# Kernel tuning notes

Hardware: AMD Instinct MI355X
Metric: run time of the kernel (lower is better)

Reference implementation:

```python
import jax, jax.numpy as jnp
import numpy as np

BS, NV, T, SD = 128, 32, 128, 64  # groups, observed vars, timesteps, state dim


def setup_inputs() -> dict:
    key = jax.random.key(0)
    k1, k2, k3, k4, k5 = jax.random.split(key, 5)
    x = jax.random.normal(k1, (BS, NV, T), jnp.float32)
    # Stable transition matrix (spectral radius < 1 so 128-step recursion is well-behaved)
    F = 0.3 * jnp.eye(SD, dtype=jnp.float32) + 0.05 * jax.random.normal(k2, (SD, SD), jnp.float32)
    H = jax.random.normal(k3, (NV, SD), jnp.float32) / jnp.sqrt(SD).astype(jnp.float32)
    A = jax.random.normal(k4, (NV, NV), jnp.float32)
    R = A @ A.T / NV + jnp.eye(NV, dtype=jnp.float32)          # SPD observation noise
    B = jax.random.normal(k5, (SD, SD), jnp.float32)
    Q = 0.1 * (B @ B.T) / SD + 0.01 * jnp.eye(SD, dtype=jnp.float32)  # SPD process noise
    return {"x": x, "F": F, "H": H, "R": R, "Q": Q}


def _kf_forward(x, F, H, R, Q):
    """forward() == predict_ahead(x, n_ahead=1) squeezed: [bs, nv, T]."""
    bs, nv, T_ = x.shape
    sd = F.shape[0]
    I = jnp.eye(sd, dtype=x.dtype)
    m0 = jnp.zeros((bs, sd), x.dtype)               # initializer: zero mean
    P0 = jnp.broadcast_to(I, (bs, sd, sd))          # initializer: identity covariance
    obs_seq = jnp.moveaxis(x, 2, 0)[: T_ - 1]       # [T-1, bs, nv]
    Ft, Ht = F.T, H.T

    def step(carry, o):
        m, P = carry                                # m: [bs,sd], P: [bs,sd,sd]
        # --- update ---
        PHt = P @ Ht                                # [bs, sd, nv]
        S = jnp.matmul(H, PHt) + R                  # [bs, nv, nv]
        resid = o - m @ Ht                          # [bs, nv]
        Sinv = jnp.linalg.inv(S)                    # batched inverse
        K = PHt @ Sinv                              # [bs, sd, nv]
        m_u = m + jnp.einsum('bsv,bv->bs', K, resid)
        p1 = I - jnp.matmul(K, H)                   # [bs, sd, sd]
        # Joseph stabilized covariance update
        P_u = p1 @ P @ p1.swapaxes(-1, -2) + (K @ R) @ K.swapaxes(-1, -2)
        # --- predict (n_ahead = 1) ---
        m_p = m_u @ Ft                              # (F @ m)
        P_p = jnp.matmul(F, P_u) @ Ft + Q
        y = m_p @ Ht                                # [bs, nv] -> output[:, :, i+1]
        return (m_p, P_p), y

    _, ys = jax.lax.scan(step, (m0, P0), obs_seq)   # ys: [T-1, bs, nv]
    out = jnp.concatenate([jnp.zeros((1, bs, nv), x.dtype), ys], axis=0)  # t=0 stays zero
    return jnp.moveaxis(out, 0, 2)                  # [bs, nv, T]


def reference(x, F, H, R, Q):
    return _kf_forward(x, F, H, R, Q)
```

## Files before the change

### kernel.cpp

```cpp
#include <hip/hip_runtime.h>


#define SD 64
#define NV 32
#define TSZ 128
#define BSZ 128
#define TMAX 120

#define MG_STRIDE (SD*SD + SD*NV)
#define WS_PAIR (120*MG_STRIDE)
#define WS_TC   (WS_PAIR + 27648)
#define OFF_M2   0
#define OFF_M3   4096
#define OFF_M4   8192
#define OFF_MG   12288
#define OFF_M2G  14336
#define OFF_M3G  16384
#define OFF_HM   18432
#define OFF_HM2  20480
#define OFF_HM3  22528
#define OFF_HG   24576
#define OFF_HMG  25600
#define OFF_HM2G 26624

#define AFB    0
#define APB    4352
#define AWB    8704
#define AHB    13056
#define AHTB   15232
#define AGRB   17536
#define AVB    19840
#define AYB    22144
#define ASIP   24320
#define ATF    25472
#define ASF    29632
#define APREVG 30688
#define AWRED  32800
#define ASZ    32808

typedef __attribute__((ext_vector_type(8))) short bf16x8;
typedef __attribute__((ext_vector_type(4))) float f32x4;

__device__ __forceinline__ unsigned packhl(float v) {
  unsigned b = __float_as_uint(v);
  unsigned hi = (b + 0x7FFFu + ((b >> 16) & 1u)) & 0xFFFF0000u;
  float lo = v - __uint_as_float(hi);
  unsigned lb = __float_as_uint(lo);
  unsigned lo16 = ((lb + 0x7FFFu + ((lb >> 16) & 1u)) >> 16);
  return hi | (lo16 & 0xFFFFu);
}

__device__ __forceinline__ void frags_from(const unsigned* __restrict__ p,
                                           bf16x8& hi, bf16x8& lo) {
  uint4 a = *(const uint4*)p;
  uint4 b = *(const uint4*)(p + 4);
  unsigned u0=a.x,u1=a.y,u2=a.z,u3=a.w,u4=b.x,u5=b.y,u6=b.z,u7=b.w;
  hi[0]=(short)(u0>>16); hi[1]=(short)(u1>>16); hi[2]=(short)(u2>>16); hi[3]=(short)(u3>>16);
  hi[4]=(short)(u4>>16); hi[5]=(short)(u5>>16); hi[6]=(short)(u6>>16); hi[7]=(short)(u7>>16);
  lo[0]=(short)(u0&0xFFFFu); lo[1]=(short)(u1&0xFFFFu); lo[2]=(short)(u2&0xFFFFu); lo[3]=(short)(u3&0xFFFFu);
  lo[4]=(short)(u4&0xFFFFu); lo[5]=(short)(u5&0xFFFFu); lo[6]=(short)(u6&0xFFFFu); lo[7]=(short)(u7&0xFFFFu);
}
// ... 12 lines not shown
__device__ __forceinline__ float rdlane(float v, int lane) {
  return __uint_as_float(
      (unsigned)__builtin_amdgcn_readlane((int)__float_as_uint(v), lane));
}

__device__ const int DE0[5][8] = {
  {APB, AWB, OFF_M2, 64, 2, 16, AFB,  1},
  {AWB, APB, -1,     64, 2, 16, AHTB, 1},
  {APB, AYB, OFF_MG, 32, 1, 8,  ATF,  2},
  {AHB, AWB, OFF_HM, 64, 2, 8,  AVB,  1},
  {AHB, AYB, OFF_HG, 32, 1, 4,  -1,   0},
};
__device__ const int DE1[8][8] = {
  {AFB, AWB,  OFF_M3,   64, 2, 16, -1, 0},
  {AFB, AHTB, OFF_M4,   64, 2, 16, -1, 0},
  {AFB, AYB,  OFF_M2G,  32, 1, 8,  -1, 0},
  {AFB, ATF,  OFF_M3G,  32, 1, 8,  -1, 0},
  {AVB, AWB,  OFF_HM2,  64, 2, 8,  -1, 0},
  {AVB, AHTB, OFF_HM3,  64, 2, 8,  -1, 0},
  {AVB, AYB,  OFF_HMG,  32, 1, 4,  -1, 0},
  {AVB, ATF,  OFF_HM2G, 32, 1, 4,  -1, 0},
};

__device__ __forceinline__ void run_desc(const int (*D)[8], int nD, int totT,
                                         unsigned* U, float* M2o,
                                         int w, int l16, int quad) {
  for (int gt = w; gt < totT; gt += 8) {
    int ti = gt, di = 0;
    while (ti >= D[di][5]) { ti -= D[di][5]; ++di; }
    const int* d = D[di];
    const int nTs = d[4];
    const int m0 = (ti >> nTs) << 4, n0 = (ti & ((1 << nTs) - 1)) << 4;
    f32x4 c = {0.f, 0.f, 0.f, 0.f};
    const unsigned* ap = U + d[0] + (m0 + l16) * 68 + quad * 8;
    const unsigned* bp = U + d[1] + (n0 + l16) * 68 + quad * 8;
    c = mfma3(ap, bp, c);
    c = mfma3(ap + 32, bp + 32, c);
    const int r0 = m0 + quad * 4, cc = n0 + l16;
    if (d[2] >= 0) {
#pragma unroll
      for (int g = 0; g < 4; ++g) M2o[d[2] + (r0 + g) * d[3] + cc] = c[g];
    }
    if (d[7] == 1) {
#pragma unroll
      for (int g = 0; g < 4; ++g) U[d[6] + (r0 + g) * 68 + cc] = packhl(c[g]);
    } else if (d[7] == 2) {
      *(uint4*)(U + d[6] + cc * 68 + r0) =
          make_uint4(packhl(c[0]), packhl(c[1]), packhl(c[2]), packhl(c[3]));
    }
  }
}

__launch_bounds__(512)
__global__ void kf_phase1(const float* __restrict__ Fg,
                          const float* __restrict__ Hg,
                          const float* __restrict__ Rg,
                          const float* __restrict__ Qg,
                          float* __restrict__ ws) {
  __shared__ unsigned AR[ASZ];
  unsigned* U = AR;
  float* Ff = (float*)AR;

  const int tid = threadIdx.x;
  const int w = tid >> 6, lane = tid & 63, quad = lane >> 4, l16 = lane & 15;

  for (int s = tid; s < SD*SD; s += 512) {
    int i = s >> 6, j = s & 63;
    U[AFB + i*68 + j] = packhl(Fg[s]);
    U[APB + i*68 + j] = packhl((i == j) ? 1.0f : 0.0f);
  }
  for (int s = tid; s < NV*SD; s += 512)
    U[AHB + (s>>6)*68 + (s&63)] = packhl(Hg[s]);
  for (int s = tid; s < SD*NV; s += 512) {
    int j = s >> 5, v = s & 31;
    U[AHTB + j*36 + v] = packhl(Hg[v*SD + j]);
    Ff[APREVG + j*33 + v] = 1e30f;
  }
  __syncthreads();

  int tcv = TMAX - 1;

  for (int t = 0; t < TMAX; ++t) {
    float* Mws = ws + (size_t)t * MG_STRIDE;
    float* Gws = Mws + SD*SD;

    for (int tt = w; tt < 24; tt += 8) {
      if (tt < 8) {
        const int m0 = (tt >> 2) << 4, n0 = (tt & 3) << 4;
        f32x4 c = {0.f, 0.f, 0.f, 0.f};
        c = mfma3(U + AHB + (m0+l16)*68 +      quad*8, U + APB + (n0+l16)*68 +      quad*8, c);
        c = mfma3(U + AHB + (m0+l16)*68 + 32 + quad*8, U + APB + (n0+l16)*68 + 32 + quad*8, c);
        const int r0 = m0 + quad*4, cc = n0 + l16;
        U[AYB + (r0+0)*68 + cc] = packhl(c[0]);
        U[AYB + (r0+1)*68 + cc] = packhl(c[1]);
        U[AYB + (r0+2)*68 + cc] = packhl(c[2]);
        U[AYB + (r0+3)*68 + cc] = packhl(c[3]);
      } else {
        const int ss = tt - 8;
        const int m0 = (ss >> 2) << 4, n0 = (ss & 3) << 4;
        f32x4 c = {0.f, 0.f, 0.f, 0.f};
        c = mfma3(U + AFB + (m0+l16)*68 +      quad*8, U + APB + (n0+l16)*68 +      quad*8, c);
        c = mfma3(U + AFB + (m0+l16)*68 + 32 + quad*8, U + APB + (n0+l16)*68 + 32 + quad*8, c);
        const int r0 = m0 + quad*4, cc = n0 + l16;
        U[AWB + (r0+0)*68 + cc] = packhl(c[0]);
        U[AWB + (r0+1)*68 + cc] = packhl(c[1]);
        U[AWB + (r0+2)*68 + cc] = packhl(c[2]);
        U[AWB + (r0+3)*68 + cc] = packhl(c[3]);
      }
    }
    __syncthreads();

    for (int tt = w; tt < 12; tt += 8) {
      if (tt < 4) {
        const int m0 = (tt >> 1) << 4, n0 = (tt & 1) << 4;
        const int r0 = m0 + quad*4, cc = n0 + l16;
        f32x4 c;
        c[0] = Rg[(r0+0)*NV + cc];
        c[1] = Rg[(r0+1)*NV + cc];
        c[2] = Rg[(r0+2)*NV + cc];
        c[3] = Rg[(r0+3)*NV + cc];
        c = mfma3(U + AYB + (m0+l16)*68 +      quad*8, U + AHB + (n0+l16)*68 +      quad*8, c);
        c = mfma3(U + AYB + (m0+l16)*68 + 32 + quad*8, U + AHB + (n0+l16)*68 + 32 + quad*8, c);
        Ff[ASF + (r0+0)*33 + cc] = c[0];
        Ff[ASF + (r0+1)*33 + cc] = c[1];
        Ff[ASF + (r0+2)*33 + cc] = c[2];
        Ff[ASF + (r0+3)*33 + cc] = c[3];
      } else {
        const int ss = tt - 4;
        const int m0 = (ss >> 1) << 4, n0 = (ss & 1) << 4;
        f32x4 c = {0.f, 0.f, 0.f, 0.f};
        c = mfma3(U + AWB + (m0+l16)*68 +      quad*8, U + AHB + (n0+l16)*68 +      quad*8, c);
        c = mfma3(U + AWB + (m0+l16)*68 + 32 + quad*8, U + AHB + (n0+l16)*68 + 32 + quad*8, c);
        const int r0 = m0 + quad*4, cc = n0 + l16;
        U[AVB + (r0+0)*36 + cc] = packhl(c[0]);
        U[AVB + (r0+1)*36 + cc] = packhl(c[1]);
        U[AVB + (r0+2)*36 + cc] = packhl(c[2]);
        U[AVB + (r0+3)*36 + cc] = packhl(c[3]);
      }
    }
    __syncthreads();

    if (tid < 64) {
      const int l = tid;
      float colX[32];
      if (l < 32) {
#pragma unroll
        for (int r = 0; r < 32; ++r) colX[r] = Ff[ASF + r*33 + l];
      } else {
#pragma unroll
        for (int r = 0; r < 32; ++r) colX[r] = (r == l - 32) ? 1.0f : 0.0f;
      }
#pragma unroll
      for (int p = 0; p < 32; ++p) {
        const float piv = rdlane(colX[p], p);
        float inv = __builtin_amdgcn_rcpf(piv);
        inv = inv * (2.0f - piv * inv);
        const float rp = colX[p] * inv;
#pragma unroll
        for (int r = 0; r < 32; ++r) {
          if (r == p) continue;
          const float f = rdlane(colX[r], p);
          colX[r] -= f * rp;
        }
        colX[p] = rp;
      }
      if (l >= 32) {
        const int c = l - 32;
#pragma unroll
        for (int r = 0; r < 32; ++r)
          U[ASIP + r*36 + c] = packhl(colX[r]);
      }
    } else {
      for (int tt = w - 1; tt < 16; tt += 7) {
        const int m0 = (tt >> 2) << 4, n0 = (tt & 3) << 4;
        f32x4 c = {0.f, 0.f, 0.f, 0.f};
        c = mfma3(U + AWB + (m0+l16)*68 +      quad*8, U + AFB + (n0+l16)*68 +      quad*8, c);
        c = mfma3(U + AWB + (m0+l16)*68 + 32 + quad*8, U + AFB + (n0+l16)*68 + 32 + quad*8, c);
        const int r0 = m0 + quad*4, cc = n0 + l16;
        Ff[ATF + (r0+0)*65 + cc] = c[0];
        Ff[ATF + (r0+1)*65 + cc] = c[1];
        Ff[ATF + (r0+2)*65 + cc] = c[2];
        Ff[ATF + (r0+3)*65 + cc] = c[3];
      }
    }
    __syncthreads();

    {
      const int m0 = (w >> 1) << 4, n0 = (w & 1) << 4;
      f32x4 c = {0.f, 0.f, 0.f, 0.f};
      c = mfma3(U + AVB + (m0+l16)*36 + quad*8, U + ASIP + (n0+l16)*36 + quad*8, c);
      const int r0 = m0 + quad*4, cc = n0 + l16;
      float dmax = 0.0f;
#pragma unroll
      for (int g = 0; g < 4; ++g) {
        const float gv = c[g];
        Gws[(r0+g)*NV + cc] = gv;
        U[AGRB + (r0+g)*36 + cc] = packhl(-gv);
        dmax = fmaxf(dmax, fabsf(gv - Ff[APREVG + (r0+g)*33 + cc]));
        Ff[APREVG + (r0+g)*33 + cc] = gv;
      }
#pragma unroll
      for (int off = 32; off >= 1; off >>= 1)
        dmax = fmaxf(dmax, __shfl_xor(dmax, off));
      if (lane == 0) Ff[AWRED + w] = dmax;
    }
    __syncthreads();

    for (int tt = w; tt < 32; tt += 8) {
      if (tt < 16) {
        const int m0 = (tt >> 2) << 4, n0 = (tt & 3) << 4;
        const int r0 = m0 + quad*4, cc = n0 + l16;
        f32x4 c;
        c[0] = Fg[(r0+0)*SD + cc];
        c[1] = Fg[(r0+1)*SD + cc];
        c[2] = Fg[(r0+2)*SD + cc];
        c[3] = Fg[(r0+3)*SD + cc];
        c = mfma3(U + AGRB + (m0+l16)*36 + quad*8, U + AHTB + (n0+l16)*36 + quad*8, c);
        Mws[(r0+0)*SD + cc] = c[0];
        Mws[(r0+1)*SD + cc] = c[1];
        Mws[(r0+2)*SD + cc] = c[2];
        Mws[(r0+3)*SD + cc] = c[3];
      } else {
        const int ss = tt - 16;
        const int m0 = (ss >> 2) << 4, n0 = (ss & 3) << 4;
        const int r0 = m0 + quad*4, cc = n0 + l16;
        f32x4 c;
        c[0] = Ff[ATF + (r0+0)*65 + cc] + Qg[(r0+0)*SD + cc];
        c[1] = Ff[ATF + (r0+1)*65 + cc] + Qg[(r0+1)*SD + cc];
        c[2] = Ff[ATF + (r0+2)*65 + cc] + Qg[(r0+2)*SD + cc];
        c[3] = Ff[ATF + (r0+3)*65 + cc] + Qg[(r0+3)*SD + cc];
        c = mfma3(U + AGRB + (m0+l16)*36 + quad*8, U + AVB + (n0+l16)*36 + quad*8, c);
        U[APB + (r0+0)*68 + cc] = packhl(c[0]);
        U[APB + (r0+1)*68 + cc] = packhl(c[1]);
        U[APB + (r0+2)*68 + cc] = packhl(c[2]);
        U[APB + (r0+3)*68 + cc] = packhl(c[3]);
      }
    }
    __syncthreads();

    float cm = Ff[AWRED + 0];
#pragma unroll
    for (int k = 1; k < 8; ++k) cm = fmaxf(cm, Ff[AWRED + k]);
    if (cm < 3e-4f) { tcv = t; break; }
  }
  if (tid == 0) ((int*)ws)[WS_TC] = tcv;

  {
    const float* Mf = ws + (size_t)tcv * MG_STRIDE;
    const float* Gf = Mf + SD*SD;
    for (int s = tid; s < SD*SD; s += 512) {
      int i = s >> 6, j = s & 63;
      unsigned pk = packhl(Mf[s]);
      U[APB + i*68 + j] = pk;
      U[AWB + j*68 + i] = pk;
    }
    for (int s = tid; s < SD*NV; s += 512) {
      int i = s >> 5, v = s & 31;
      U[AYB + v*68 + i] = packhl(Gf[s]);
    }
    __syncthreads();
    float* M2o = ws + WS_PAIR;
    run_desc(DE0, 5, 52, U, M2o, w, l16, quad);
    __syncthreads();
    run_desc(DE1, 8, 72, U, M2o, w, l16, quad);
  }
}

__launch_bounds__(256)
__global__ void kf_phase2(const float* __restrict__ x,
                          const float* __restrict__ Hg,
                          const float* __restrict__ ws,
                          float* __restrict__ out) {
  __shared__ __align__(16) float Hs2[NV*65];
  __shared__ __align__(16) float xt[132*36];
  __shared__ __align__(16) float yb[NV*129];
  __shared__ __align__(16) float mbuf[2*SD];
  __shared__ __align__(16) float M4s [SD*68];
  __shared__ __align__(16) float M3Gs[SD*36];
  __shared__ __align__(16) float M2Gs[SD*36];
  __shared__ __align__(16) float MGs [SD*36];
  __shared__ __align__(16) float Gs  [SD*36];
  __shared__ __align__(16) float HMs [NV*68];
  __shared__ __align__(16) float HM2s[NV*68];
  __shared__ __align__(16) float HM3s[NV*68];
  __shared__ __align__(16) float HGs [NV*36];
  __shared__ __align__(16) float HMGs[NV*36];
  __shared__ __align__(16) float HM2Gs[NV*36];
  const int tid = threadIdx.x, b = blockIdx.x;

  const int tc = ((const int*)ws)[WS_TC];
  const float* P = ws + WS_PAIR;
  const float* Gf = ws + (size_t)tc * MG_STRIDE + SD*SD;

  for (int s = tid; s < NV*SD; s += 256) {
    int v = s >> 6, j = s & 63;
    Hs2[v*65 + j] = Hg[s];
    HMs [v*68 + j] = P[OFF_HM  + s];
    HM2s[v*68 + j] = P[OFF_HM2 + s];
    HM3s[v*68 + j] = P[OFF_HM3 + s];
  }
  for (int s = tid; s < SD*SD; s += 256) M4s[(s>>6)*68 + (s&63)] = P[OFF_M4 + s];
  for (int s = tid; s < SD*NV; s += 256) {
    int i = s >> 5, v = s & 31;
    M3Gs[i*36 + v] = P[OFF_M3G + s];
    M2Gs[i*36 + v] = P[OFF_M2G + s];
    MGs [i*36 + v] = P[OFF_MG  + s];
    Gs  [i*36 + v] = Gf[s];
  }
  for (int s = tid; s < NV*NV; s += 256) {
    int v = s >> 5, u = s & 31;
    HGs  [v*36 + u] = P[OFF_HG   + s];
    HMGs [v*36 + u] = P[OFF_HMG  + s];
    HM2Gs[v*36 + u] = P[OFF_HM2G + s];
  }
  for (int s = tid; s < 4*36; s += 256) xt[128*36 + s] = 0.0f;
  for (int s = tid; s < NV*TSZ; s += 256) {
    int v = s >> 7, t = s & 127;
    xt[t*36 + v] = x[(size_t)b*NV*TSZ + s];
  }
  if (tid < NV) yb[tid*129] = 0.0f;
  if (tid < 2*SD) mbuf[tid] = 0.0f;
  __syncthreads();

  const int i = tid >> 2, p4 = tid & 3;
  const int v = tid >> 3, p8 = tid & 7;
  int cb = 0;

  for (int t = 0; t < tc; ++t) {
    const float* Mt = ws + (size_t)t * MG_STRIDE;
    const float* Gt = Mt + SD*SD;
    const float* cur = mbuf + cb * SD;
    float*       nxt = mbuf + (cb ^ 1) * SD;

    float acc = 0.0f;
    {
      const int j0 = p4 * 16;
#pragma unroll
      for (int c = 0; c < 16; c += 4) {
        float4 mm = *(const float4*)(Mt + i*SD + j0 + c);
        float4 vv = *(const float4*)(cur + j0 + c);
        acc += mm.x*vv.x + mm.y*vv.y + mm.z*vv.z + mm.w*vv.w;
      }
      const int v0 = p4 * 8;
#pragma unroll
      for (int c = 0; c < 8; c += 4) {
        float4 gg = *(const float4*)(Gt + i*NV + v0 + c);
        float4 oo = *(const float4*)(xt + t*36 + v0 + c);
        acc += gg.x*oo.x + gg.y*oo.y + gg.z*oo.z + gg.w*oo.w;
      }
    }
    acc += __shfl_xor(acc, 1);
    acc += __shfl_xor(acc, 2);

    if (t >= 1) {
      float ys = 0.0f;
#pragma unroll
      for (int j = 0; j < 8; ++j)
        ys += Hs2[v*65 + p8*8 + j] * cur[p8*8 + j];
      ys += __shfl_xor(ys, 1);
      ys += __shfl_xor(ys, 2);
      ys += __shfl_xor(ys, 4);
      if (p8 == 0) yb[v*129 + t] = ys;
    }
    if (p4 == 0) nxt[i] = acc;
    __syncthreads();
    cb ^= 1;
  }

  for (int t = tc; t < TSZ; t += 4) {
    const float* cur = mbuf + cb * SD;
    float*       nxt = mbuf + (cb ^ 1) * SD;
    const float* o0 = xt + t*36;
    const float* o1 = o0 + 36;
    const float* o2 = o1 + 36;
    const float* o3 = o2 + 36;

    {
      const int j8 = p8 * 8, j4 = p8 * 4;
      float y0 = 0.f, y1 = 0.f, y2 = 0.f, y3 = 0.f;
#pragma unroll
      for (int c = 0; c < 8; c += 4) {
        float4 vv = *(const float4*)(cur + j8 + c);
        float4 h0 = *(const float4*)(Hs2 + v*65 + j8 + c);
        float4 h1 = *(const float4*)(HMs + v*68 + j8 + c);
        float4 h2 = *(const float4*)(HM2s + v*68 + j8 + c);
        float4 h3 = *(const float4*)(HM3s + v*68 + j8 + c);
        y0 += h0.x*vv.x + h0.y*vv.y + h0.z*vv.z + h0.w*vv.w;
        y1 += h1.x*vv.x + h1.y*vv.y + h1.z*vv.z + h1.w*vv.w;
        y2 += h2.x*vv.x + h2.y*vv.y + h2.z*vv.z + h2.w*vv.w;
        y3 += h3.x*vv.x + h3.y*vv.y + h3.z*vv.z + h3.w*vv.w;
      }
      {
        float4 a = *(const float4*)(HGs + v*36 + j4);
        float4 bq = *(const float4*)(HMGs + v*36 + j4);
        float4 cq = *(const float4*)(HM2Gs + v*36 + j4);
        float4 q0 = *(const float4*)(o0 + j4);
        float4 q1 = *(const float4*)(o1 + j4);
        float4 q2 = *(const float4*)(o2 + j4);
        y1 += a.x*q0.x + a.y*q0.y + a.z*q0.z + a.w*q0.w;
        y2 += bq.x*q0.x + bq.y*q0.y + bq.z*q0.z + bq.w*q0.w
            + a.x*q1.x + a.y*q1.y + a.z*q1.z + a.w*q1.w;
        y3 += cq.x*q0.x + cq.y*q0.y + cq.z*q0.z + cq.w*q0.w
            + bq.x*q1.x + bq.y*q1.y + bq.z*q1.z + bq.w*q1.w
            + a.x*q2.x + a.y*q2.y + a.z*q2.z + a.w*q2.w;
      }
#pragma unroll
      for (int off = 1; off <= 4; off <<= 1) {
        y0 += __shfl_xor(y0, off);
        y1 += __shfl_xor(y1, off);
        y2 += __shfl_xor(y2, off);
        y3 += __shfl_xor(y3, off);
      }
      if (p8 == 0) {
        yb[v*129 + t] = y0;
        if (t + 1 < TSZ) yb[v*129 + t + 1] = y1;
        if (t + 2 < TSZ) yb[v*129 + t + 2] = y2;
        if (t + 3 < TSZ) yb[v*129 + t + 3] = y3;
      }
    }

    {
      float acc = 0.0f;
      const int j0 = p4 * 16;
#pragma unroll
      for (int c = 0; c < 16; c += 4) {
        float4 mm = *(const float4*)(M4s + i*68 + j0 + c);
        float4 vv = *(const float4*)(cur + j0 + c);
        acc += mm.x*vv.x + mm.y*vv.y + mm.z*vv.z + mm.w*vv.w;
      }
      const int v0 = p4 * 8;
#pragma unroll
      for (int c = 0; c < 8; c += 4) {
        float4 g3 = *(const float4*)(M3Gs + i*36 + v0 + c);
        float4 g2 = *(const float4*)(M2Gs + i*36 + v0 + c);
        float4 g1 = *(const float4*)(MGs + i*36 + v0 + c);
        float4 g0 = *(const float4*)(Gs + i*36 + v0 + c);
        float4 q0 = *(const float4*)(o0 + v0 + c);
        float4 q1 = *(const float4*)(o1 + v0 + c);
        float4 q2 = *(const float4*)(o2 + v0 + c);
        float4 q3 = *(const float4*)(o3 + v0 + c);
        acc += g3.x*q0.x + g3.y*q0.y + g3.z*q0.z + g3.w*q0.w;
        acc += g2.x*q1.x + g2.y*q1.y + g2.z*q1.z + g2.w*q1.w;
        acc += g1.x*q2.x + g1.y*q2.y + g1.z*q2.z + g1.w*q2.w;
        acc += g0.x*q3.x + g0.y*q3.y + g0.z*q3.z + g0.w*q3.w;
      }
      acc += __shfl_xor(acc, 1);
      acc += __shfl_xor(acc, 2);
      if (p4 == 0) nxt[i] = acc;
    }
    __syncthreads();
    cb ^= 1;
  }

  for (int s = tid; s < NV*TSZ; s += 256)
    out[(size_t)b*NV*TSZ + s] = yb[(s>>7)*129 + (s&127)];
}

extern "C" void kernel_launch(void* const* d_in, const int* in_sizes, int n_in,
                              void* d_out, int out_size, void* d_ws, size_t ws_size,
                              hipStream_t stream) {
  const float* x = (const float*)d_in[0];
  const float* F = (const float*)d_in[1];
  const float* H = (const float*)d_in[2];
  const float* R = (const float*)d_in[3];
  const float* Q = (const float*)d_in[4];
  float* out = (float*)d_out;
  float* ws  = (float*)d_ws;

  hipLaunchKernelGGL(kf_phase1, dim3(1), dim3(512), 0, stream, F, H, R, Q, ws);
  hipLaunchKernelGGL(kf_phase2, dim3(BSZ), dim3(256), 0, stream, x, H, ws, out);
}
```

Measured before the change: 199.3 us.

## Fuse gain-precompute and batch filter kernels with flag-based producer-consumer overlap

Merges the single-block covariance/gain kernel and the per-batch mean-recursion kernel into one launch of 129 blocks. Block 0 computes the gain sequence and publishes progress through a release-store flag in workspace, while the other 128 blocks spin on that flag and consume each step's M/G as soon as it is written. This overlaps the serial Riccati recursion with the batch mean updates and removes a kernel launch boundary. It relies on all 129 blocks being co-resident to avoid deadlock, and it adds spin-wait and global fence overhead. The Gauss-Jordan inverse loop is also reworked to a rotating-register form with unroll 1, which shrinks code size.

```diff
diff --git a/kernel.cpp b/kernel.cpp
--- a/kernel.cpp
+++ b/kernel.cpp
@@ -4,12 +4,11 @@
 #define SD 64
 #define NV 32
 #define TSZ 128
-#define BSZ 128
 #define TMAX 120
 
 #define MG_STRIDE (SD*SD + SD*NV)
 #define WS_PAIR (120*MG_STRIDE)
-#define WS_TC   (WS_PAIR + 27648)
+#define WS_FLAG (WS_PAIR + 27648)
 #define OFF_M2   0
 #define OFF_M3   4096
 #define OFF_M4   8192
@@ -36,7 +35,24 @@
 #define ASF    29632
 #define APREVG 30688
 #define AWRED  32800
-#define ASZ    32808
+
+#define P2_HS2  0
+#define P2_XT   2080
+#define P2_YB   6832
+#define P2_MB   10960
+#define P2_M4   11088
+#define P2_M3G  15440
+#define P2_M2G  17744
+#define P2_MG   20048
+#define P2_G    22352
+#define P2_HM   24656
+#define P2_HM2  26832
+#define P2_HM3  29008
+#define P2_HG   31184
+#define P2_HMG  32336
+#define P2_HM2G 33488
+#define P2_FLG  34640
+#define ASZ2    34644
 
 typedef __attribute__((ext_vector_type(8))) short bf16x8;
 typedef __attribute__((ext_vector_type(4))) float f32x4;
@@ -95,7 +111,7 @@
   {AVB, ATF,  OFF_HM2G, 32, 1, 4,  -1, 0},
 };
 
-__device__ __forceinline__ void run_desc(const int (*D)[8], int nD, int totT,
+__device__ __forceinline__ void run_desc(const int (*D)[8], int totT,
                                          unsigned* U, float* M2o,
                                          int w, int l16, int quad) {
   for (int gt = w; gt < totT; gt += 8) {
@@ -125,408 +141,428 @@
 }
 
 __launch_bounds__(512)
-__global__ void kf_phase1(const float* __restrict__ Fg,
-                          const float* __restrict__ Hg,
-                          const float* __restrict__ Rg,
-                          const float* __restrict__ Qg,
-                          float* __restrict__ ws) {
-  __shared__ unsigned AR[ASZ];
-  unsigned* U = AR;
-  float* Ff = (float*)AR;
-
+__global__ void kf_fused(const float* __restrict__ x,
+                         const float* __restrict__ Fg,
+                         const float* __restrict__ Hg,
+                         const float* __restrict__ Rg,
+                         const float* __restrict__ Qg,
+                         float* __restrict__ out,
+                         float* __restrict__ ws) {
+  __shared__ unsigned AR[ASZ2];
   const int tid = threadIdx.x;
   const int w = tid >> 6, lane = tid & 63, quad = lane >> 4, l16 = lane & 15;
-
-  for (int s = tid; s < SD*SD; s += 512) {
-    int i = s >> 6, j = s & 63;
-    U[AFB + i*68 + j] = packhl(Fg[s]);
-    U[APB + i*68 + j] = packhl((i == j) ? 1.0f : 0.0f);
-  }
-  for (int s = tid; s < NV*SD; s += 512)
-    U[AHB + (s>>6)*68 + (s&63)] = packhl(Hg[s]);
-  for (int s = tid; s < SD*NV; s += 512) {
-    int j = s >> 5, v = s & 31;
-    U[AHTB + j*36 + v] = packhl(Hg[v*SD + j]);
-    Ff[APREVG + j*33 + v] = 1e30f;
-  }
-  __syncthreads();
-
-  int tcv = TMAX - 1;
-
-  for (int t = 0; t < TMAX; ++t) {
-    float* Mws = ws + (size_t)t * MG_STRIDE;
-    float* Gws = Mws + SD*SD;
-
-    for (int tt = w; tt < 24; tt += 8) {
-      if (tt < 8) {
-        const int m0 = (tt >> 2) << 4, n0 = (tt & 3) << 4;
-        f32x4 c = {0.f, 0.f, 0.f, 0.f};
-        c = mfma3(U + AHB + (m0+l16)*68 +      quad*8, U + APB + (n0+l16)*68 +      quad*8, c);
-        c = mfma3(U + AHB + (m0+l16)*68 + 32 + quad*8, U + APB + (n0+l16)*68 + 32 + quad*8, c);
-        const int r0 = m0 + quad*4, cc = n0 + l16;
-        U[AYB + (r0+0)*68 + cc] = packhl(c[0]);
-        U[AYB + (r0+1)*68 + cc] = packhl(c[1]);
-        U[AYB + (r0+2)*68 + cc] = packhl(c[2]);
-        U[AYB + (r0+3)*68 + cc] = packhl(c[3]);
-      } else {
-        const int ss = tt - 8;
-        const int m0 = (ss >> 2) << 4, n0 = (ss & 3) << 4;
-        f32x4 c = {0.f, 0.f, 0.f, 0.f};
-        c = mfma3(U + AFB + (m0+l16)*68 +      quad*8, U + APB + (n0+l16)*68 +      quad*8, c);
-        c = mfma3(U + AFB + (m0+l16)*68 + 32 + quad*8, U + APB + (n0+l16)*68 + 32 + quad*8, c);
-        const int r0 = m0 + quad*4, cc = n0 + l16;
-        U[AWB + (r0+0)*68 + cc] = packhl(c[0]);
-        U[AWB + (r0+1)*68 + cc] = packhl(c[1]);
-        U[AWB + (r0+2)*68 + cc] = packhl(c[2]);
-        U[AWB + (r0+3)*68 + cc] = packhl(c[3]);
-      }
-    }
-    __syncthreads();
-
-    for (int tt = w; tt < 12; tt += 8) {
-      if (tt < 4) {
-        const int m0 = (tt >> 1) << 4, n0 = (tt & 1) << 4;
-        const int r0 = m0 + quad*4, cc = n0 + l16;
-        f32x4 c;
-        c[0] = Rg[(r0+0)*NV + cc];
-        c[1] = Rg[(r0+1)*NV + cc];
-        c[2] = Rg[(r0+2)*NV + cc];
-        c[3] = Rg[(r0+3)*NV + cc];
-        c = mfma3(U + AYB + (m0+l16)*68 +      quad*8, U + AHB + (n0+l16)*68 +      quad*8, c);
-        c = mfma3(U + AYB + (m0+l16)*68 + 32 + quad*8, U + AHB + (n0+l16)*68 + 32 + quad*8, c);
-        Ff[ASF + (r0+0)*33 + cc] = c[0];
-        Ff[ASF + (r0+1)*33 + cc] = c[1];
-        Ff[ASF + (r0+2)*33 + cc] = c[2];
-        Ff[ASF + (r0+3)*33 + cc] = c[3];
-      } else {
-        const int ss = tt - 4;
-        const int m0 = (ss >> 1) << 4, n0 = (ss & 1) << 4;
-        f32x4 c = {0.f, 0.f, 0.f, 0.f};
-        c = mfma3(U + AWB + (m0+l16)*68 +      quad*8, U + AHB + (n0+l16)*68 +      quad*8, c);
-        c = mfma3(U + AWB + (m0+l16)*68 + 32 + quad*8, U + AHB + (n0+l16)*68 + 32 + quad*8, c);
-        const int r0 = m0 + quad*4, cc = n0 + l16;
-        U[AVB + (r0+0)*36 + cc] = packhl(c[0]);
-        U[AVB + (r0+1)*36 + cc] = packhl(c[1]);
-        U[AVB + (r0+2)*36 + cc] = packhl(c[2]);
-        U[AVB + (r0+3)*36 + cc] = packhl(c[3]);
-      }
-    }
-    __syncthreads();
-
-    if (tid < 64) {
-      const int l = tid;
-      float colX[32];
-      if (l < 32) {
-#pragma unroll
-        for (int r = 0; r < 32; ++r) colX[r] = Ff[ASF + r*33 + l];
-      } else {
-#pragma unroll
-        for (int r = 0; r < 32; ++r) colX[r] = (r == l - 32) ? 1.0f : 0.0f;
-      }
-#pragma unroll
-      for (int p = 0; p < 32; ++p) {
-        const float piv = rdlane(colX[p], p);
-        float inv = __builtin_amdgcn_rcpf(piv);
-        inv = inv * (2.0f - piv * inv);
-        const float rp = colX[p] * inv;
-#pragma unroll
-        for (int r = 0; r < 32; ++r) {
-          if (r == p) continue;
-          const float f = rdlane(colX[r], p);
-          colX[r] -= f * rp;
-        }
-        colX[p] = rp;
-      }
-      if (l >= 32) {
-        const int c = l - 32;
-#pragma unroll
-        for (int r = 0; r < 32; ++r)
-          U[ASIP + r*36 + c] = packhl(colX[r]);
-      }
-    } else {
-      for (int tt = w - 1; tt < 16; tt += 7) {
-        const int m0 = (tt >> 2) << 4, n0 = (tt & 3) << 4;
-        f32x4 c = {0.f, 0.f, 0.f, 0.f};
-        c = mfma3(U + AWB + (m0+l16)*68 +      quad*8, U + AFB + (n0+l16)*68 +      quad*8, c);
-        c = mfma3(U + AWB + (m0+l16)*68 + 32 + quad*8, U + AFB + (n0+l16)*68 + 32 + quad*8, c);
-        const int r0 = m0 + quad*4, cc = n0 + l16;
-        Ff[ATF + (r0+0)*65 + cc] = c[0];
-        Ff[ATF + (r0+1)*65 + cc] = c[1];
-        Ff[ATF + (r0+2)*65 + cc] = c[2];
-        Ff[ATF + (r0+3)*65 + cc] = c[3];
-      }
-    }
-    __syncthreads();
-
-    {
-      const int m0 = (w >> 1) << 4, n0 = (w & 1) << 4;
-      f32x4 c = {0.f, 0.f, 0.f, 0.f};
-      c = mfma3(U + AVB + (m0+l16)*36 + quad*8, U + ASIP + (n0+l16)*36 + quad*8, c);
-      const int r0 = m0 + quad*4, cc = n0 + l16;
-      float dmax = 0.0f;
-#pragma unroll
-      for (int g = 0; g < 4; ++g) {
-        const float gv = c[g];
-        Gws[(r0+g)*NV + cc] = gv;
-        U[AGRB + (r0+g)*36 + cc] = packhl(-gv);
-        dmax = fmaxf(dmax, fabsf(gv - Ff[APREVG + (r0+g)*33 + cc]));
-        Ff[APREVG + (r0+g)*33 + cc] = gv;
-      }
-#pragma unroll
-      for (int off = 32; off >= 1; off >>= 1)
-        dmax = fmaxf(dmax, __shfl_xor(dmax, off));
-      if (lane == 0) Ff[AWRED + w] = dmax;
-    }
-    __syncthreads();
-
-    for (int tt = w; tt < 32; tt += 8) {
-      if (tt < 16) {
-        const int m0 = (tt >> 2) << 4, n0 = (tt & 3) << 4;
-        const int r0 = m0 + quad*4, cc = n0 + l16;
-        f32x4 c;
-        c[0] = Fg[(r0+0)*SD + cc];
-        c[1] = Fg[(r0+1)*SD + cc];
-        c[2] = Fg[(r0+2)*SD + cc];
-        c[3] = Fg[(r0+3)*SD + cc];
-        c = mfma3(U + AGRB + (m0+l16)*36 + quad*8, U + AHTB + (n0+l16)*36 + quad*8, c);
-        Mws[(r0+0)*SD + cc] = c[0];
-        Mws[(r0+1)*SD + cc] = c[1];
-        Mws[(r0+2)*SD + cc] = c[2];
-        Mws[(r0+3)*SD + cc] = c[3];
-      } else {
-        const int ss = tt - 16;
-        const int m0 = (ss >> 2) << 4, n0 = (ss & 3) << 4;
-        const int r0 = m0 + quad*4, cc = n0 + l16;
-        f32x4 c;
-        c[0] = Ff[ATF + (r0+0)*65 + cc] + Qg[(r0+0)*SD + cc];
-        c[1] = Ff[ATF + (r0+1)*65 + cc] + Qg[(r0+1)*SD + cc];
-        c[2] = Ff[ATF + (r0+2)*65 + cc] + Qg[(r0+2)*SD + cc];
-        c[3] = Ff[ATF + (r0+3)*65 + cc] + Qg[(r0+3)*SD + cc];
-        c = mfma3(U + AGRB + (m0+l16)*36 + quad*8, U + AVB + (n0+l16)*36 + quad*8, c);
-        U[APB + (r0+0)*68 + cc] = packhl(c[0]);
-        U[APB + (r0+1)*68 + cc] = packhl(c[1]);
-        U[APB + (r0+2)*68 + cc] = packhl(c[2]);
-        U[APB + (r0+3)*68 + cc] = packhl(c[3]);
-      }
-    }
-    __syncthreads();
-
-    float cm = Ff[AWRED + 0];
-#pragma unroll
-    for (int k = 1; k < 8; ++k) cm = fmaxf(cm, Ff[AWRED + k]);
-    if (cm < 3e-4f) { tcv = t; break; }
-  }
-  if (tid == 0) ((int*)ws)[WS_TC] = tcv;
-
-  {
-    const float* Mf = ws + (size_t)tcv * MG_STRIDE;
-    const float* Gf = Mf + SD*SD;
+  int* flagp = (int*)ws + WS_FLAG;
+
+  if (blockIdx.x == 0) {
+    unsigned* U = AR;
+    float* Ff = (float*)AR;
+
     for (int s = tid; s < SD*SD; s += 512) {
       int i = s >> 6, j = s & 63;
-      unsigned pk = packhl(Mf[s]);
-      U[APB + i*68 + j] = pk;
-      U[AWB + j*68 + i] = pk;
-    }
+      U[AFB + i*68 + j] = packhl(Fg[s]);
+      U[APB + i*68 + j] = packhl((i == j) ? 1.0f : 0.0f);
+    }
+    for (int s = tid; s < NV*SD; s += 512)
+      U[AHB + (s>>6)*68 + (s&63)] = packhl(Hg[s]);
     for (int s = tid; s < SD*NV; s += 512) {
-      int i = s >> 5, v = s & 31;
-      U[AYB + v*68 + i] = packhl(Gf[s]);
+      int j = s >> 5, v = s & 31;
+      U[AHTB + j*36 + v] = packhl(Hg[v*SD + j]);
+      Ff[APREVG + j*33 + v] = 1e30f;
     }
     __syncthreads();
-    float* M2o = ws + WS_PAIR;
-    run_desc(DE0, 5, 52, U, M2o, w, l16, quad);
+
+    int tcv = TMAX - 1;
+
+    for (int t = 0; t < TMAX; ++t) {
+      float* Mws = ws + (size_t)t * MG_STRIDE;
+      float* Gws = Mws + SD*SD;
+
+      for (int tt = w; tt < 24; tt += 8) {
+        if (tt < 8) {
+          const int m0 = (tt >> 2) << 4, n0 = (tt & 3) << 4;
+          f32x4 c = {0.f, 0.f, 0.f, 0.f};
+          c = mfma3(U + AHB + (m0+l16)*68 +      quad*8, U + APB + (n0+l16)*68 +      quad*8, c);
+          c = mfma3(U + AHB + (m0+l16)*68 + 32 + quad*8, U + APB + (n0+l16)*68 + 32 + quad*8, c);
+          const int r0 = m0 + quad*4, cc = n0 + l16;
+          U[AYB + (r0+0)*68 + cc] = packhl(c[0]);
+          U[AYB + (r0+1)*68 + cc] = packhl(c[1]);
+          U[AYB + (r0+2)*68 + cc] = packhl(c[2]);
+          U[AYB + (r0+3)*68 + cc] = packhl(c[3]);
+        } else {
+          const int ss = tt - 8;
+          const int m0 = (ss >> 2) << 4, n0 = (ss & 3) << 4;
+          f32x4 c = {0.f, 0.f, 0.f, 0.f};
+          c = mfma3(U + AFB + (m0+l16)*68 +      quad*8, U + APB + (n0+l16)*68 +      quad*8, c);
+          c = mfma3(U + AFB + (m0+l16)*68 + 32 + quad*8, U + APB + (n0+l16)*68 + 32 + quad*8, c);
+          const int r0 = m0 + quad*4, cc = n0 + l16;
+          U[AWB + (r0+0)*68 + cc] = packhl(c[0]);
+          U[AWB + (r0+1)*68 + cc] = packhl(c[1]);
+          U[AWB + (r0+2)*68 + cc] = packhl(c[2]);
+          U[AWB + (r0+3)*68 + cc] = packhl(c[3]);
+        }
+      }
+      __syncthreads();
+
+      for (int tt = w; tt < 12; tt += 8) {
+        if (tt < 4) {
+          const int m0 = (tt >> 1) << 4, n0 = (tt & 1) << 4;
+          const int r0 = m0 + quad*4, cc = n0 + l16;
+          f32x4 c;
+          c[0] = Rg[(r0+0)*NV + cc];
+          c[1] = Rg[(r0+1)*NV + cc];
+          c[2] = Rg[(r0+2)*NV + cc];
+          c[3] = Rg[(r0+3)*NV + cc];
+          c = mfma3(U + AYB + (m0+l16)*68 +      quad*8, U + AHB + (n0+l16)*68 +      quad*8, c);
+          c = mfma3(U + AYB + (m0+l16)*68 + 32 + quad*8, U + AHB + (n0+l16)*68 + 32 + quad*8, c);
+          Ff[ASF + (r0+0)*33 + cc] = c[0];
+          Ff[ASF + (r0+1)*33 + cc] = c[1];
+          Ff[ASF + (r0+2)*33 + cc] = c[2];
+          Ff[ASF + (r0+3)*33 + cc] = c[3];
+        } else {
+          const int ss = tt - 4;
+          const int m0 = (ss >> 1) << 4, n0 = (ss & 1) << 4;
+          f32x4 c = {0.f, 0.f, 0.f, 0.f};
+          c = mfma3(U + AWB + (m0+l16)*68 +      quad*8, U + AHB + (n0+l16)*68 +      quad*8, c);
+          c = mfma3(U + AWB + (m0+l16)*68 + 32 + quad*8, U + AHB + (n0+l16)*68 + 32 + quad*8, c);
+          const int r0 = m0 + quad*4, cc = n0 + l16;
+          U[AVB + (r0+0)*36 + cc] = packhl(c[0]);
+          U[AVB + (r0+1)*36 + cc] = packhl(c[1]);
+          U[AVB + (r0+2)*36 + cc] = packhl(c[2]);
+          U[AVB + (r0+3)*36 + cc] = packhl(c[3]);
+        }
+      }
+      __syncthreads();
+
+      if (tid < 64) {
+        const int l = tid;
+        float cur[32];
+        if (l < 32) {
+#pragma unroll
+          for (int r = 0; r < 32; ++r) cur[r] = Ff[ASF + r*33 + l];
+        } else {
+#pragma unroll
+          for (int r = 0; r < 32; ++r) cur[r] = (r == l - 32) ? 1.0f : 0.0f;
+        }
+#pragma unroll 1
+        for (int p = 0; p < 32; ++p) {
+          const float piv = rdlane(cur[0], p);
+          float inv = __builtin_amdgcn_rcpf(piv);
+          inv = inv * (2.0f - piv * inv);
+          const float rp = cur[0] * inv;
+#pragma unroll
+          for (int r = 1; r < 32; ++r) {
+            const float f = rdlane(cur[r], p);
+            cur[r-1] = cur[r] - f * rp;
+          }
+          cur[31] = rp;
+        }
+        if (l >= 32) {
+          const int c = l - 32;
+#pragma unroll
+          for (int r = 0; r < 32; ++r)
+            U[ASIP + r*36 + c] = packhl(cur[r]);
+        }
+      } else {
+        for (int tt = w - 1; tt < 16; tt += 7) {
+          const int m0 = (tt >> 2) << 4, n0 = (tt & 3) << 4;
+          f32x4 c = {0.f, 0.f, 0.f, 0.f};
+          c = mfma3(U + AWB + (m0+l16)*68 +      quad*8, U + AFB + (n0+l16)*68 +      quad*8, c);
+          c = mfma3(U + AWB + (m0+l16)*68 + 32 + quad*8, U + AFB + (n0+l16)*68 + 32 + quad*8, c);
+          const int r0 = m0 + quad*4, cc = n0 + l16;
+          Ff[ATF + (r0+0)*65 + cc] = c[0];
+          Ff[ATF + (r0+1)*65 + cc] = c[1];
+          Ff[ATF + (r0+2)*65 + cc] = c[2];
+          Ff[ATF + (r0+3)*65 + cc] = c[3];
+        }
+      }
+      __syncthreads();
+
+      {
+        const int m0 = (w >> 1) << 4, n0 = (w & 1) << 4;
+        f32x4 c = {0.f, 0.f, 0.f, 0.f};
+        c = mfma3(U + AVB + (m0+l16)*36 + quad*8, U + ASIP + (n0+l16)*36 + quad*8, c);
+        const int r0 = m0 + quad*4, cc = n0 + l16;
+        float dmax = 0.0f;
+#pragma unroll
+        for (int g = 0; g < 4; ++g) {
+          const float gv = c[g];
+          Gws[(r0+g)*NV + cc] = gv;
+          U[AGRB + (r0+g)*36 + cc] = packhl(-gv);
+          dmax = fmaxf(dmax, fabsf(gv - Ff[APREVG + (r0+g)*33 + cc]));
+          Ff[APREVG + (r0+g)*33 + cc] = gv;
+        }
+#pragma unroll
+        for (int off = 32; off >= 1; off >>= 1)
+          dmax = fmaxf(dmax, __shfl_xor(dmax, off));
+        if (lane == 0) Ff[AWRED + w] = dmax;
+      }
+      __syncthreads();
+
+      for (int tt = w; tt < 32; tt += 8) {
+        if (tt < 16) {
+          const int m0 = (tt >> 2) << 4, n0 = (tt & 3) << 4;
+          const int r0 = m0 + quad*4, cc = n0 + l16;
+          f32x4 c;
+          c[0] = Fg[(r0+0)*SD + cc];
+          c[1] = Fg[(r0+1)*SD + cc];
+          c[2] = Fg[(r0+2)*SD + cc];
+          c[3] = Fg[(r0+3)*SD + cc];
+          c = mfma3(U + AGRB + (m0+l16)*36 + quad*8, U + AHTB + (n0+l16)*36 + quad*8, c);
+          Mws[(r0+0)*SD + cc] = c[0];
+          Mws[(r0+1)*SD + cc] = c[1];
+          Mws[(r0+2)*SD + cc] = c[2];
+          Mws[(r0+3)*SD + cc] = c[3];
+        } else {
+          const int ss = tt - 16;
+          const int m0 = (ss >> 2) << 4, n0 = (ss & 3) << 4;
+          const int r0 = m0 + quad*4, cc = n0 + l16;
+          f32x4 c;
+          c[0] = Ff[ATF + (r0+0)*65 + cc] + Qg[(r0+0)*SD + cc];
+          c[1] = Ff[ATF + (r0+1)*65 + cc] + Qg[(r0+1)*SD + cc];
+          c[2] = Ff[ATF + (r0+2)*65 + cc] + Qg[(r0+2)*SD + cc];
+          c[3] = Ff[ATF + (r0+3)*65 + cc] + Qg[(r0+3)*SD + cc];
+          c = mfma3(U + AGRB + (m0+l16)*36 + quad*8, U + AVB + (n0+l16)*36 + quad*8, c);
+          U[APB + (r0+0)*68 + cc] = packhl(c[0]);
+          U[APB + (r0+1)*68 + cc] = packhl(c[1]);
+          U[APB + (r0+2)*68 + cc] = packhl(c[2]);
+          U[APB + (r0+3)*68 + cc] = packhl(c[3]);
+        }
+      }
+      __threadfence();
+      __syncthreads();
+      if (tid == 0)
+        __hip_atomic_store(flagp, t + 1, __ATOMIC_RELEASE, __HIP_MEMORY_SCOPE_AGENT);
+
+      float cm = Ff[AWRED + 0];
+#pragma unroll
+      for (int k = 1; k < 8; ++k) cm = fmaxf(cm, Ff[AWRED + k]);
+      if (cm < 3e-4f) { tcv = t; break; }
+    }
+
+    {
+      const float* Mf = ws + (size_t)tcv * MG_STRIDE;
+      const float* Gf = Mf + SD*SD;
+      unsigned* U2 = AR;
+      for (int s = tid; s < SD*SD; s += 512) {
+        int i = s >> 6, j = s & 63;
+        unsigned pk = packhl(Mf[s]);
+        U2[APB + i*68 + j] = pk;
+        U2[AWB + j*68 + i] = pk;
+      }
+      for (int s = tid; s < SD*NV; s += 512) {
+        int i = s >> 5, v = s & 31;
+        U2[AYB + v*68 + i] = packhl(Gf[s]);
+      }
+      __syncthreads();
+      float* M2o = ws + WS_PAIR;
+      run_desc(DE0, 52, U2, M2o, w, l16, quad);
+      __syncthreads();
+      run_desc(DE1, 72, U2, M2o, w, l16, quad);
+      __threadfence();
+      __syncthreads();
+      if (tid == 0)
+        __hip_atomic_store(flagp, 1000 + tcv, __ATOMIC_RELEASE, __HIP_MEMORY_SCOPE_AGENT);
+    }
+    return;
+  }
+
+  {
+    const int b = blockIdx.x - 1;
+    float* S = (float*)AR;
+    float* Hs2 = S + P2_HS2;
+    float* xt  = S + P2_XT;
+    float* yb  = S + P2_YB;
+    float* mbuf = S + P2_MB;
+    const float* P = ws + WS_PAIR;
+
+    for (int s = tid; s < NV*SD; s += 512)
+      Hs2[(s>>6)*65 + (s&63)] = Hg[s];
+    for (int s = tid; s < 4*36; s += 512) xt[128*36 + s] = 0.0f;
+    for (int s = tid; s < NV*TSZ; s += 512) {
+      int v = s >> 7, t0 = s & 127;
+      xt[t0*36 + v] = x[(size_t)b*NV*TSZ + s];
+    }
+    if (tid < NV) yb[tid*129] = 0.0f;
+    if (tid < 2*SD) mbuf[tid] = 0.0f;
     __syncthreads();
-    run_desc(DE1, 8, 72, U, M2o, w, l16, quad);
+
+    const int i = tid >> 2, p4 = tid & 3;
+    const int v = tid >> 3, p8 = tid & 7;
+    int cb = 0, t = 0, tc;
+
+    for (;;) {
+      if (tid == 0) {
+        int fv;
+        for (;;) {
+          fv = __hip_atomic_load(flagp, __ATOMIC_ACQUIRE, __HIP_MEMORY_SCOPE_AGENT);
+          if (fv >= t + 1 || fv >= 1000) break;
+          __builtin_amdgcn_s_sleep(8);
+        }
+        ((int*)AR)[P2_FLG] = fv;
+      }
+      __syncthreads();
+      const int f = ((int*)AR)[P2_FLG];
+      __threadfence();
+      if (f >= 1000 && t >= f - 1000) { tc = f - 1000; break; }
+
+      if (tid < 256) {
+        const float* Mt = ws + (size_t)t * MG_STRIDE;
+        const float* Gt = Mt + SD*SD;
+        const float* cur = mbuf + cb * SD;
+        float*       nxt = mbuf + (cb ^ 1) * SD;
+
+        float acc = 0.0f;
+        {
+          const int j0 = p4 * 16;
+#pragma unroll
+          for (int c = 0; c < 16; c += 4) {
+            float4 mm = *(const float4*)(Mt + i*SD + j0 + c);
+            float4 vv = *(const float4*)(cur + j0 + c);
+            acc += mm.x*vv.x + mm.y*vv.y + mm.z*vv.z + mm.w*vv.w;
+          }
+          const int v0 = p4 * 8;
+#pragma unroll
+          for (int c = 0; c < 8; c += 4) {
+            float4 gg = *(const float4*)(Gt + i*NV + v0 + c);
+            float4 oo = *(const float4*)(xt + t*36 + v0 + c);
+            acc += gg.x*oo.x + gg.y*oo.y + gg.z*oo.z + gg.w*oo.w;
+          }
+        }
+        acc += __shfl_xor(acc, 1);
+        acc += __shfl_xor(acc, 2);
+
+        if (t >= 1) {
+          float ys = 0.0f;
+#pragma unroll
+          for (int j = 0; j < 8; ++j)
+            ys += Hs2[v*65 + p8*8 + j] * cur[p8*8 + j];
+          ys += __shfl_xor(ys, 1);
+          ys += __shfl_xor(ys, 2);
+          ys += __shfl_xor(ys, 4);
+          if (p8 == 0) yb[v*129 + t] = ys;
+        }
+        if (p4 == 0) nxt[i] = acc;
+      }
+      __syncthreads();
+      cb ^= 1; ++t;
+    }
+
+    {
+      const float* Gf = ws + (size_t)tc * MG_STRIDE + SD*SD;
+      for (int s = tid; s < NV*SD; s += 512) {
+        int vv = s >> 6, j = s & 63;
+        S[P2_HM  + vv*68 + j] = P[OFF_HM  + s];
+        S[P2_HM2 + vv*68 + j] = P[OFF_HM2 + s];
+        S[P2_HM3 + vv*68 + j] = P[OFF_HM3 + s];
+      }
+      for (int s = tid; s < SD*SD; s += 512)
+        S[P2_M4 + (s>>6)*68 + (s&63)] = P[OFF_M4 + s];
+      for (int s = tid; s < SD*NV; s += 512) {
+        int ii = s >> 5, vv = s & 31;
+        S[P2_M3G + ii*36 + vv] = P[OFF_M3G + s];
+        S[P2_M2G + ii*36 + vv] = P[OFF_M2G + s];
+        S[P2_MG  + ii*36 + vv] = P[OFF_MG  + s];
+        S[P2_G   + ii*36 + vv] = Gf[s];
+      }
+      for (int s = tid; s < NV*NV; s += 512) {
+        int vv = s >> 5, u = s & 31;
+        S[P2_HG   + vv*36 + u] = P[OFF_HG   + s];
+        S[P2_HMG  + vv*36 + u] = P[OFF_HMG  + s];
+        S[P2_HM2G + vv*36 + u] = P[OFF_HM2G + s];
+      }
+    }
+    __syncthreads();
+
+    for (; t < TSZ; t += 4) {
+      if (tid < 256) {
+        const float* cur = mbuf + cb * SD;
+        float*       nxt = mbuf + (cb ^ 1) * SD;
+        const float* o0 = xt + t*36;
+        const float* o1 = o0 + 36;
+        const float* o2 = o1 + 36;
+        const float* o3 = o2 + 36;
+
+        {
+          const int j8 = p8 * 8, j4 = p8 * 4;
+          float y0 = 0.f, y1 = 0.f, y2 = 0.f, y3 = 0.f;
+#pragma unroll
+          for (int c = 0; c < 8; c += 4) {
+            float4 vv = *(const float4*)(cur + j8 + c);
+            float4 h0 = *(const float4*)(Hs2 + v*65 + j8 + c);
+            float4 h1 = *(const float4*)(S + P2_HM  + v*68 + j8 + c);
+            float4 h2 = *(const float4*)(S + P2_HM2 + v*68 + j8 + c);
+            float4 h3 = *(const float4*)(S + P2_HM3 + v*68 + j8 + c);
+            y0 += h0.x*vv.x + h0.y*vv.y + h0.z*vv.z + h0.w*vv.w;
+            y1 += h1.x*vv.x + h1.y*vv.y + h1.z*vv.z + h1.w*vv.w;
+            y2 += h2.x*vv.x + h2.y*vv.y + h2.z*vv.z + h2.w*vv.w;
+            y3 += h3.x*vv.x + h3.y*vv.y + h3.z*vv.z + h3.w*vv.w;
+          }
+          {
+            float4 a  = *(const float4*)(S + P2_HG   + v*36 + j4);
+            float4 bq = *(const float4*)(S + P2_HMG  + v*36 + j4);
+            float4 cq = *(const float4*)(S + P2_HM2G + v*36 + j4);
+            float4 q0 = *(const float4*)(o0 + j4);
+            float4 q1 = *(const float4*)(o1 + j4);
+            float4 q2 = *(const float4*)(o2 + j4);
+            y1 += a.x*q0.x + a.y*q0.y + a.z*q0.z + a.w*q0.w;
+            y2 += bq.x*q0.x + bq.y*q0.y + bq.z*q0.z + bq.w*q0.w
+                + a.x*q1.x + a.y*q1.y + a.z*q1.z + a.w*q1.w;
+            y3 += cq.x*q0.x + cq.y*q0.y + cq.z*q0.z + cq.w*q0.w
+                + bq.x*q1.x + bq.y*q1.y + bq.z*q1.z + bq.w*q1.w
+                + a.x*q2.x + a.y*q2.y + a.z*q2.z + a.w*q2.w;
+          }
+#pragma unroll
+          for (int off = 1; off <= 4; off <<= 1) {
+            y0 += __shfl_xor(y0, off);
+            y1 += __shfl_xor(y1, off);
+            y2 += __shfl_xor(y2, off);
+            y3 += __shfl_xor(y3, off);
+          }
+          if (p8 == 0) {
+            yb[v*129 + t] = y0;
+            if (t + 1 < TSZ) yb[v*129 + t + 1] = y1;
+            if (t + 2 < TSZ) yb[v*129 + t + 2] = y2;
+            if (t + 3 < TSZ) yb[v*129 + t + 3] = y3;
+          }
+        }
+
+        {
+          float acc = 0.0f;
+          const int j0 = p4 * 16;
+#pragma unroll
+          for (int c = 0; c < 16; c += 4) {
+            float4 mm = *(const float4*)(S + P2_M4 + i*68 + j0 + c);
+            float4 vv = *(const float4*)(cur + j0 + c);
+            acc += mm.x*vv.x + mm.y*vv.y + mm.z*vv.z + mm.w*vv.w;
+          }
+          const int v0 = p4 * 8;
+#pragma unroll
+          for (int c = 0; c < 8; c += 4) {
+            float4 g3 = *(const float4*)(S + P2_M3G + i*36 + v0 + c);
+            float4 g2 = *(const float4*)(S + P2_M2G + i*36 + v0 + c);
+            float4 g1 = *(const float4*)(S + P2_MG  + i*36 + v0 + c);
+            float4 g0 = *(const float4*)(S + P2_G   + i*36 + v0 + c);
+            float4 q0 = *(const float4*)(o0 + v0 + c);
+            float4 q1 = *(const float4*)(o1 + v0 + c);
+            float4 q2 = *(const float4*)(o2 + v0 + c);
+            float4 q3 = *(const float4*)(o3 + v0 + c);
+            acc += g3.x*q0.x + g3.y*q0.y + g3.z*q0.z + g3.w*q0.w;
+            acc += g2.x*q1.x + g2.y*q1.y + g2.z*q1.z + g2.w*q1.w;
+            acc += g1.x*q2.x + g1.y*q2.y + g1.z*q2.z + g1.w*q2.w;
+            acc += g0.x*q3.x + g0.y*q3.y + g0.z*q3.z + g0.w*q3.w;
+          }
+          acc += __shfl_xor(acc, 1);
+          acc += __shfl_xor(acc, 2);
+          if (p4 == 0) nxt[i] = acc;
+        }
+      }
+      __syncthreads();
+      cb ^= 1;
+    }
+
+    for (int s = tid; s < NV*TSZ; s += 512)
+      out[(size_t)b*NV*TSZ + s] = yb[(s>>7)*129 + (s&127)];
   }
-}
-
-__launch_bounds__(256)
-__global__ void kf_phase2(const float* __restrict__ x,
-                          const float* __restrict__ Hg,
-                          const float* __restrict__ ws,
-                          float* __restrict__ out) {
-  __shared__ __align__(16) float Hs2[NV*65];
-  __shared__ __align__(16) float xt[132*36];
-  __shared__ __align__(16) float yb[NV*129];
-  __shared__ __align__(16) float mbuf[2*SD];
-  __shared__ __align__(16) float M4s [SD*68];
-  __shared__ __align__(16) float M3Gs[SD*36];
-  __shared__ __align__(16) float M2Gs[SD*36];
-  __shared__ __align__(16) float MGs [SD*36];
-  __shared__ __align__(16) float Gs  [SD*36];
-  __shared__ __align__(16) float HMs [NV*68];
-  __shared__ __align__(16) float HM2s[NV*68];
-  __shared__ __align__(16) float HM3s[NV*68];
-  __shared__ __align__(16) float HGs [NV*36];
-  __shared__ __align__(16) float HMGs[NV*36];
-  __shared__ __align__(16) float HM2Gs[NV*36];
-  const int tid = threadIdx.x, b = blockIdx.x;
-
-  const int tc = ((const int*)ws)[WS_TC];
-  const float* P = ws + WS_PAIR;
-  const float* Gf = ws + (size_t)tc * MG_STRIDE + SD*SD;
-
-  for (int s = tid; s < NV*SD; s += 256) {
-    int v = s >> 6, j = s & 63;
-    Hs2[v*65 + j] = Hg[s];
-    HMs [v*68 + j] = P[OFF_HM  + s];
-    HM2s[v*68 + j] = P[OFF_HM2 + s];
-    HM3s[v*68 + j] = P[OFF_HM3 + s];
-  }
-  for (int s = tid; s < SD*SD; s += 256) M4s[(s>>6)*68 + (s&63)] = P[OFF_M4 + s];
-  for (int s = tid; s < SD*NV; s += 256) {
-    int i = s >> 5, v = s & 31;
-    M3Gs[i*36 + v] = P[OFF_M3G + s];
-    M2Gs[i*36 + v] = P[OFF_M2G + s];
-    MGs [i*36 + v] = P[OFF_MG  + s];
-    Gs  [i*36 + v] = Gf[s];
-  }
-  for (int s = tid; s < NV*NV; s += 256) {
-    int v = s >> 5, u = s & 31;
-    HGs  [v*36 + u] = P[OFF_HG   + s];
-    HMGs [v*36 + u] = P[OFF_HMG  + s];
-    HM2Gs[v*36 + u] = P[OFF_HM2G + s];
-  }
-  for (int s = tid; s < 4*36; s += 256) xt[128*36 + s] = 0.0f;
-  for (int s = tid; s < NV*TSZ; s += 256) {
-    int v = s >> 7, t = s & 127;
-    xt[t*36 + v] = x[(size_t)b*NV*TSZ + s];
-  }
-  if (tid < NV) yb[tid*129] = 0.0f;
-  if (tid < 2*SD) mbuf[tid] = 0.0f;
-  __syncthreads();
-
-  const int i = tid >> 2, p4 = tid & 3;
-  const int v = tid >> 3, p8 = tid & 7;
-  int cb = 0;
-
-  for (int t = 0; t < tc; ++t) {
-    const float* Mt = ws + (size_t)t * MG_STRIDE;
-    const float* Gt = Mt + SD*SD;
-    const float* cur = mbuf + cb * SD;
-    float*       nxt = mbuf + (cb ^ 1) * SD;
-
-    float acc = 0.0f;
-    {
-      const int j0 = p4 * 16;
-#pragma unroll
-      for (int c = 0; c < 16; c += 4) {
-        float4 mm = *(const float4*)(Mt + i*SD + j0 + c);
-        float4 vv = *(const float4*)(cur + j0 + c);
-        acc += mm.x*vv.x + mm.y*vv.y + mm.z*vv.z + mm.w*vv.w;
-      }
-      const int v0 = p4 * 8;
-#pragma unroll
-      for (int c = 0; c < 8; c += 4) {
-        float4 gg = *(const float4*)(Gt + i*NV + v0 + c);
-        float4 oo = *(const float4*)(xt + t*36 + v0 + c);
-        acc += gg.x*oo.x + gg.y*oo.y + gg.z*oo.z + gg.w*oo.w;
-      }
-    }
-    acc += __shfl_xor(acc, 1);
-    acc += __shfl_xor(acc, 2);
-
-    if (t >= 1) {
-      float ys = 0.0f;
-#pragma unroll
-      for (int j = 0; j < 8; ++j)
-        ys += Hs2[v*65 + p8*8 + j] * cur[p8*8 + j];
-      ys += __shfl_xor(ys, 1);
-      ys += __shfl_xor(ys, 2);
-      ys += __shfl_xor(ys, 4);
-      if (p8 == 0) yb[v*129 + t] = ys;
-    }
-    if (p4 == 0) nxt[i] = acc;
-    __syncthreads();
-    cb ^= 1;
-  }
-
-  for (int t = tc; t < TSZ; t += 4) {
-    const float* cur = mbuf + cb * SD;
-    float*       nxt = mbuf + (cb ^ 1) * SD;
-    const float* o0 = xt + t*36;
-    const float* o1 = o0 + 36;
-    const float* o2 = o1 + 36;
-    const float* o3 = o2 + 36;
-
-    {
-      const int j8 = p8 * 8, j4 = p8 * 4;
-      float y0 = 0.f, y1 = 0.f, y2 = 0.f, y3 = 0.f;
-#pragma unroll
-      for (int c = 0; c < 8; c += 4) {
-        float4 vv = *(const float4*)(cur + j8 + c);
-        float4 h0 = *(const float4*)(Hs2 + v*65 + j8 + c);
-        float4 h1 = *(const float4*)(HMs + v*68 + j8 + c);
-        float4 h2 = *(const float4*)(HM2s + v*68 + j8 + c);
-        float4 h3 = *(const float4*)(HM3s + v*68 + j8 + c);
-        y0 += h0.x*vv.x + h0.y*vv.y + h0.z*vv.z + h0.w*vv.w;
-        y1 += h1.x*vv.x + h1.y*vv.y + h1.z*vv.z + h1.w*vv.w;
-        y2 += h2.x*vv.x + h2.y*vv.y + h2.z*vv.z + h2.w*vv.w;
-        y3 += h3.x*vv.x + h3.y*vv.y + h3.z*vv.z + h3.w*vv.w;
-      }
-      {
-        float4 a = *(const float4*)(HGs + v*36 + j4);
-        float4 bq = *(const float4*)(HMGs + v*36 + j4);
-        float4 cq = *(const float4*)(HM2Gs + v*36 + j4);
-        float4 q0 = *(const float4*)(o0 + j4);
-        float4 q1 = *(const float4*)(o1 + j4);
-        float4 q2 = *(const float4*)(o2 + j4);
-        y1 += a.x*q0.x + a.y*q0.y + a.z*q0.z + a.w*q0.w;
-        y2 += bq.x*q0.x + bq.y*q0.y + bq.z*q0.z + bq.w*q0.w
-            + a.x*q1.x + a.y*q1.y + a.z*q1.z + a.w*q1.w;
-        y3 += cq.x*q0.x + cq.y*q0.y + cq.z*q0.z + cq.w*q0.w
-            + bq.x*q1.x + bq.y*q1.y + bq.z*q1.z + bq.w*q1.w
-            + a.x*q2.x + a.y*q2.y + a.z*q2.z + a.w*q2.w;
-      }
-#pragma unroll
-      for (int off = 1; off <= 4; off <<= 1) {
-        y0 += __shfl_xor(y0, off);
-        y1 += __shfl_xor(y1, off);
-        y2 += __shfl_xor(y2, off);
-        y3 += __shfl_xor(y3, off);
-      }
-      if (p8 == 0) {
-        yb[v*129 + t] = y0;
-        if (t + 1 < TSZ) yb[v*129 + t + 1] = y1;
-        if (t + 2 < TSZ) yb[v*129 + t + 2] = y2;
-        if (t + 3 < TSZ) yb[v*129 + t + 3] = y3;
-      }
-    }
-
-    {
-      float acc = 0.0f;
-      const int j0 = p4 * 16;
-#pragma unroll
-      for (int c = 0; c < 16; c += 4) {
-        float4 mm = *(const float4*)(M4s + i*68 + j0 + c);
-        float4 vv = *(const float4*)(cur + j0 + c);
-        acc += mm.x*vv.x + mm.y*vv.y + mm.z*vv.z + mm.w*vv.w;
-      }
-      const int v0 = p4 * 8;
-#pragma unroll
-      for (int c = 0; c < 8; c += 4) {
-        float4 g3 = *(const float4*)(M3Gs + i*36 + v0 + c);
-        float4 g2 = *(const float4*)(M2Gs + i*36 + v0 + c);
-        float4 g1 = *(const float4*)(MGs + i*36 + v0 + c);
-        float4 g0 = *(const float4*)(Gs + i*36 + v0 + c);
-        float4 q0 = *(const float4*)(o0 + v0 + c);
-        float4 q1 = *(const float4*)(o1 + v0 + c);
-        float4 q2 = *(const float4*)(o2 + v0 + c);
-        float4 q3 = *(const float4*)(o3 + v0 + c);
-        acc += g3.x*q0.x + g3.y*q0.y + g3.z*q0.z + g3.w*q0.w;
-        acc += g2.x*q1.x + g2.y*q1.y + g2.z*q1.z + g2.w*q1.w;
-        acc += g1.x*q2.x + g1.y*q2.y + g1.z*q2.z + g1.w*q2.w;
-        acc += g0.x*q3.x + g0.y*q3.y + g0.z*q3.z + g0.w*q3.w;
-      }
-      acc += __shfl_xor(acc, 1);
-      acc += __shfl_xor(acc, 2);
-      if (p4 == 0) nxt[i] = acc;
-    }
-    __syncthreads();
-    cb ^= 1;
-  }
-
-  for (int s = tid; s < NV*TSZ; s += 256)
-    out[(size_t)b*NV*TSZ + s] = yb[(s>>7)*129 + (s&127)];
 }
 
 extern "C" void kernel_launch(void* const* d_in, const int* in_sizes, int n_in,
@@ -540,6 +576,6 @@
   float* out = (float*)d_out;
   float* ws  = (float*)d_ws;
 
-  hipLaunchKernelGGL(kf_phase1, dim3(1), dim3(512), 0, stream, F, H, R, Q, ws);
-  hipLaunchKernelGGL(kf_phase2, dim3(BSZ), dim3(256), 0, stream, x, H, ws, out);
-}
+  hipLaunchKernelGGL(kf_fused, dim3(129), dim3(512), 0, stream,
+                     x, F, H, R, Q, out, ws);
+}
```

New measurement: 373.9 us. 87.6% more time.
